# Kernel optimization log

Hardware: AMD Instinct MI355X
Metric: run time of the kernel (lower is better)

The kernel has to match this reference:

```python
import jax, jax.numpy as jnp
import numpy as np

HEADS = 6
POINTS = 4
INJ_SHAPES = ((96, 96), (48, 48), (24, 24))  # adapter pyramid (H_l, W_l), sum = 12096 tokens
EXT_SHAPES = ((48, 48),)                      # vit grid level


def layernorm(x, g, b, eps=1e-6):
    m = jnp.mean(x, axis=-1, keepdims=True)
    v = jnp.mean((x - m) ** 2, axis=-1, keepdims=True)
    return (x - m) * jax.lax.rsqrt(v + eps) * g + b


def bilinear_sample(img, loc):
    # img: [B, heads, H, W, D]; loc: [B, heads, P, 2] normalized (x, y) in [0, 1]
    # matches F.grid_sample(mode='bilinear', padding_mode='zeros', align_corners=False)
    B, nh, H, W, D = img.shape
    flat = img.reshape(B, nh, H * W, D)
    ix = loc[..., 0] * W - 0.5
    iy = loc[..., 1] * H - 0.5
    x0f = jnp.floor(ix)
    y0f = jnp.floor(iy)
    wx = (ix - x0f)[..., None]
    wy = (iy - y0f)[..., None]
    x0 = x0f.astype(jnp.int32)
    y0 = y0f.astype(jnp.int32)

    def gather(xi, yi):
        valid = (xi >= 0) & (xi < W) & (yi >= 0) & (yi < H)
        idx = jnp.clip(yi, 0, H - 1) * W + jnp.clip(xi, 0, W - 1)
        g = jnp.take_along_axis(flat, idx[..., None], axis=2)
        return g * valid[..., None]

    v00 = gather(x0, y0)
    v01 = gather(x0 + 1, y0)
    v10 = gather(x0, y0 + 1)
    v11 = gather(x0 + 1, y0 + 1)
    return (v00 * (1 - wx) + v01 * wx) * (1 - wy) + (v10 * (1 - wx) + v11 * wx) * wy


def msda(query, value, ref, shapes, Wv, bv, Ws, bs_, Wa, ba, Wo, bo):
    # mmcv MultiScaleDeformableAttention (batch_first) without dropout/identity.
    B, Lq, C = query.shape
    D = C // HEADS
    L = len(shapes)
    v = (value @ Wv + bv).reshape(B, -1, HEADS, D)
    off = (query @ Ws + bs_).reshape(B, Lq, HEADS, L, POINTS, 2)
    aw = jax.nn.softmax((query @ Wa + ba).reshape(B, Lq, HEADS, L * POINTS), axis=-1)
    aw = aw.reshape(B, Lq, HEADS, L, POINTS)
    norm = jnp.array([[w, h] for (h, w) in shapes], dtype=query.dtype)  # (x, y) normalizer
    # ref: [B, Lq, 1, 2] broadcasts over heads/levels/points
    loc = ref[:, :, None, :, None, :] + off / norm[None, None, None, :, None, :]
    starts = np.cumsum([0] + [h * w for h, w in shapes])
    out = jnp.zeros((B, HEADS, Lq, D), query.dtype)
    for l, (h, w) in enumerate(shapes):
        vl = v[:, starts[l]:starts[l + 1]].reshape(B, h, w, HEADS, D).transpose(0, 3, 1, 2, 4)
        ll = loc[:, :, :, l].transpose(0, 2, 1, 3, 4).reshape(B, HEADS, Lq * POINTS, 2)
        s = bilinear_sample(vl, ll).reshape(B, HEADS, Lq, POINTS, D)
        out = out + jnp.einsum('bhqp,bhqpd->bhqd', aw[:, :, :, l].transpose(0, 2, 1, 3), s)
    out = out.transpose(0, 2, 1, 3).reshape(B, Lq, C)
    return out @ Wo + bo


def setup_inputs() -> dict:
    key = jax.random.key(0)
    ks = jax.random.split(key, 24)
    B, Hh, Ww, C = 1, 48, 48, 768
    NA = 12096  # 4*HW + HW + HW/4
    f32 = jnp.float32
    lin = lambda k, i, o, s=0.02: jax.random.normal(k, (i, o), f32) * s
    p = {
        'vit_feats': jax.random.normal(ks[0], (B, Hh, Ww, C), f32),
        'adapter_feats': jax.random.normal(ks[1], (B, NA, C), f32),
        'ref1': jax.random.uniform(ks[2], (B, Hh * Ww, 1, 2), f32),
        'ref2': jax.random.uniform(ks[3], (B, NA, 1, 2), f32),
        'inj_qn_g': jnp.ones((C,), f32), 'inj_qn_b': jnp.zeros((C,), f32),
        'inj_Wv': lin(ks[4], C, C), 'inj_bv': jnp.zeros((C,), f32),
        'inj_Ws': lin(ks[5], C, HEADS * 3 * POINTS * 2, 0.01),
        'inj_bs': jax.random.normal(ks[6], (HEADS * 3 * POINTS * 2,), f32),
        'inj_Wa': lin(ks[7], C, HEADS * 3 * POINTS), 'inj_ba': jnp.zeros((HEADS * 3 * POINTS,), f32),
        'inj_Wo': lin(ks[8], C, C), 'inj_bo': jnp.zeros((C,), f32),
        'inj_gamma': jax.random.normal(ks[9], (C,), f32) * 0.1,
        'ext_vn_g': jnp.ones((C,), f32), 'ext_vn_b': jnp.zeros((C,), f32),
        'ext_qn_g': jnp.ones((C,), f32), 'ext_qn_b': jnp.zeros((C,), f32),
        'ext_Wv': lin(ks[10], C, C), 'ext_bv': jnp.zeros((C,), f32),
        'ext_Ws': lin(ks[11], C, HEADS * 1 * POINTS * 2, 0.01),
        'ext_bs': jax.random.normal(ks[12], (HEADS * 1 * POINTS * 2,), f32),
        'ext_Wa': lin(ks[13], C, HEADS * 1 * POINTS), 'ext_ba': jnp.zeros((HEADS * 1 * POINTS,), f32),
        'ext_Wo': lin(ks[14], C, C), 'ext_bo': jnp.zeros((C,), f32),
        'H': 48, 'W': 48,
    }
    return p


def reference(vit_feats, adapter_feats, ref1, ref2,
              inj_qn_g, inj_qn_b, inj_Wv, inj_bv, inj_Ws, inj_bs, inj_Wa, inj_ba, inj_Wo, inj_bo, inj_gamma,
              ext_vn_g, ext_vn_b, ext_qn_g, ext_qn_b, ext_Wv, ext_bv, ext_Ws, ext_bs, ext_Wa, ext_ba, ext_Wo, ext_bo,
              H, W):
    b, h, w, c = vit_feats.shape
    q = vit_feats.reshape(b, h * w, c)
    # Injector: query = vit tokens, value = 3-level adapter pyramid; identity = 0, gamma-scaled residual
    attn = msda(layernorm(q, inj_qn_g, inj_qn_b), adapter_feats, ref1, INJ_SHAPES,
                inj_Wv, inj_bv, inj_Ws, inj_bs, inj_Wa, inj_ba, inj_Wo, inj_bo)
    q = q + inj_gamma * attn
    vit_out = q.reshape(b, h, w, c)
    # Extractor (with_cffn=False, v_pre_norm=True): value = LN(vit tokens), identity = adapter query, post query-norm
    value = layernorm(q, ext_vn_g, ext_vn_b)
    attn2 = msda(adapter_feats, value, ref2, EXT_SHAPES,
                 ext_Wv, ext_bv, ext_Ws, ext_bs, ext_Wa, ext_ba, ext_Wo, ext_bo)
    adapter_out = layernorm(adapter_feats + attn2, ext_qn_g, ext_qn_b)
    return vit_out, adapter_out
```

## Files before the change

kernel.cpp:

```cpp
#include <hip/hip_runtime.h>


#define LQ_VIT 2304
#define NA_ADA 12096

typedef float f32x4 __attribute__((ext_vector_type(4)));
typedef short bf16x8 __attribute__((ext_vector_type(8)));

__device__ __forceinline__ unsigned short f2bf(float f) {
  unsigned u = __builtin_bit_cast(unsigned, f);
  u += 0x7FFFu + ((u >> 16) & 1u);
  return (unsigned short)(u >> 16);
}
__device__ __forceinline__ float bf2f(unsigned short u) {
  return __builtin_bit_cast(float, (unsigned)u << 16);
}
__device__ __forceinline__ f32x4 ld4bf(const unsigned short* p) {
  ushort4 t = *(const ushort4*)p;
  f32x4 r; r[0] = bf2f(t.x); r[1] = bf2f(t.y); r[2] = bf2f(t.z); r[3] = bf2f(t.w);
  return r;
}

__device__ __forceinline__ void gload_lds16(const void* g, void* l) {
  __builtin_amdgcn_global_load_lds(
      (__attribute__((address_space(1))) void*)(void*)g,
      (__attribute__((address_space(3))) void*)l, 16, 0, 0);
}

#define FENCE() __builtin_amdgcn_sched_barrier(0)

struct PrepPack {
  const float* W[8];
  unsigned short* WT[8];
  int N[8];
  int cum[9];
  const float* adapter; unsigned short* adbf; int n4;
  const float* vit; const float* qg; const float* qb; unsigned short* qln;
  const float* isv; const float* iav; const float* ibv;
  const float* esv; const float* eav;
  float* bci; float* bbig;
};

__global__ __launch_bounds__(256) void prep_kernel(PrepPack pp) {
  int b = blockIdx.x;
  int tid = threadIdx.x;
  if (b < 2568) {
    int kb = b / 107, col = b % 107;
    int z = 0;
#pragma unroll
    for (int i = 0; i < 8; i++) if (col >= pp.cum[i + 1]) z = i + 1;
    int nb = col - pp.cum[z];
    const float* __restrict__ W = pp.W[z];
    unsigned short* __restrict__ WT = pp.WT[z];
    int N = pp.N[z];
    int kb32 = kb * 32, nb32 = nb * 32;
    __shared__ float tile[32][33];
    int tx = tid & 31, ty = tid >> 5;
    for (int i = ty; i < 32; i += 8) {
      int n = nb32 + tx;
      tile[i][tx] = (n < N) ? W[(size_t)(kb32 + i) * N + n] : 0.f;
    }
    __syncthreads();
    for (int i = ty; i < 32; i += 8) {
      int n = nb32 + i, k = kb32 + tx;
      if (n < N) WT[(size_t)n * 768 + k] = f2bf(tile[tx][i]);
    }
  } else if (b < 4616) {
    for (int i = (b - 2568) * 256 + tid; i < pp.n4; i += 2048 * 256) {
      float4 v = ((const float4*)pp.adapter)[i];
      ushort4 o;
      o.x = f2bf(v.x); o.y = f2bf(v.y); o.z = f2bf(v.z); o.w = f2bf(v.w);
      ((ushort4*)pp.adbf)[i] = o;
    }
  } else if (b < 5192) {
    int wid = (b - 4616) * 4 + (tid >> 6);
    int lane = tid & 63;
    if (wid >= LQ_VIT) return;
    const float* row = pp.vit + (size_t)wid * 768;
    float x[12]; float s = 0.f;
#pragma unroll
    for (int j = 0; j < 12; j++) { x[j] = row[lane + j * 64]; s += x[j]; }
#pragma unroll
    for (int o = 32; o >= 1; o >>= 1) s += __shfl_xor(s, o);
    float mean = s * (1.f / 768.f);
    float v = 0.f;
#pragma unroll
    for (int j = 0; j < 12; j++) { float d = x[j] - mean; v += d * d; }
#pragma unroll
    for (int o = 32; o >= 1; o >>= 1) v += __shfl_xor(v, o);
    float rs = rsqrtf(v * (1.f / 768.f) + 1e-6f);
#pragma unroll
    for (int j = 0; j < 12; j++) {
      int c = lane + j * 64;
      pp.qln[(size_t)wid * 768 + c] = f2bf((x[j] - mean) * rs * pp.qg[c] + pp.qb[c]);
    }
  } else {
    for (int i = tid; i < 840; i += 256) {
      if (i < 144) pp.bci[i] = pp.isv[i];
      else if (i < 216) pp.bci[i] = pp.iav[i - 144];
      if (i < 768) pp.bbig[i] = pp.ibv[i];
      else if (i < 816) pp.bbig[i] = pp.esv[i - 768];
      else pp.bbig[i] = pp.eav[i - 816];
    }
  }
}

struct GemmTask {
  const unsigned short* A; const unsigned short* BT;
  const float* bias; unsigned short* C;
  int M, N, NT, nwg;
};

__global__ __launch_bounds__(256) void gemm_big_kernel(GemmTask t0, GemmTask t1, int split) {
  __shared__ unsigned short lds[3][(128 + 128) * 32];

  GemmTask tk = (blockIdx.x < split) ? t0 : t1;
  int id = (blockIdx.x < split) ? blockIdx.x : blockIdx.x - split;
  int nwg = tk.nwg;
  int qq = nwg >> 3, rr = nwg & 7;
  int xcd = id & 7, idx = id >> 3;
  int wg = (xcd < rr ? xcd * (qq + 1) : rr * (qq + 1) + (xcd - rr) * qq) + idx;
  int nt = wg % tk.NT, mt = wg / tk.NT;
  int m0 = mt * 128, n0 = nt * 128;
  int M = tk.M, N = tk.N;
  const unsigned short* __restrict__ A = tk.A;
  const unsigned short* __restrict__ BT = tk.BT;
  const int K = 768, kT = 24;

  int tid = threadIdx.x;
  int w = tid >> 6, lane = tid & 63;
  int wr = w >> 1, wc = w & 1;
  int frow = lane & 15, ghi = lane >> 4;
  int sr = lane >> 2;
  int sgx = (((lane & 3) ^ ((lane >> 3) & 3)) * 8);
  int gxr = ((ghi ^ ((frow >> 1) & 3)) * 8);

  f32x4 acc[4][4] = {};

  auto stage = [&](unsigned short* dst, int k0) {
#pragma unroll
    for (int i = 0; i < 4; i++) {
      int c = w * 4 + i;
      if (c < 8) {
        int gm = m0 + c * 16 + sr; if (gm >= M) gm = M - 1;
        gload_lds16(&A[(size_t)gm * K + k0 + sgx], &dst[c * 512]);
      } else {
        int gn = n0 + (c - 8) * 16 + sr; if (gn >= N) gn = N - 1;
        gload_lds16(&BT[(size_t)gn * K + k0 + sgx], &dst[c * 512]);
      }
    }
  };

  stage(&lds[0][0], 0);
  stage(&lds[1][0], 32);
  asm volatile("s_waitcnt vmcnt(4)" ::: "memory");
  FENCE();
  __builtin_amdgcn_s_barrier();
  FENCE();

#pragma unroll
  for (int t = 0; t < kT; t++) {
    unsigned short* cb = &lds[t % 3][0];
    if (t + 2 < kT) stage(&lds[(t + 2) % 3][0], (t + 2) << 5);
    const unsigned short* As_ = cb;
    const unsigned short* Bs_ = cb + 128 * 32;
    bf16x8 af[4], bg[4];
#pragma unroll
    for (int m = 0; m < 4; m++)
      af[m] = *(const bf16x8*)&As_[(wr * 64 + m * 16 + frow) * 32 + gxr];
#pragma unroll
    for (int n = 0; n < 4; n++)
      bg[n] = *(const bf16x8*)&Bs_[(wc * 64 + n * 16 + frow) * 32 + gxr];
#pragma unroll
    for (int m = 0; m < 4; m++)
#pragma unroll
      for (int n = 0; n < 4; n++)
        acc[m][n] = __builtin_amdgcn_mfma_f32_16x16x32_bf16(af[m], bg[n], acc[m][n], 0, 0, 0);
    if (t < kT - 1) {
      if (t + 2 < kT) { asm volatile("s_waitcnt vmcnt(4)" ::: "memory"); }
      else            { asm volatile("s_waitcnt vmcnt(0)" ::: "memory"); }
      FENCE();
      __builtin_amdgcn_s_barrier();
      FENCE();
    }
  }

  int orow = (lane >> 4) * 4, ocol = lane & 15;
  unsigned short* C = tk.C;
  const float* bias = tk.bias;
#pragma unroll
  for (int m = 0; m < 4; m++) {
    int gmb = m0 + wr * 64 + m * 16 + orow;
#pragma unroll
    for (int n = 0; n < 4; n++) {
      int gn = n0 + wc * 64 + n * 16 + ocol;
      if (gn < N) {
        float bv = bias[gn];
#pragma unroll
        for (int r = 0; r < 4; r++) {
          int gm = gmb + r;
          if (gm < M) C[(size_t)gm * N + gn] = f2bf(acc[m][n][r] + bv);
        }
      }
    }
  }
}

__global__ __launch_bounds__(256) void gemm_mid_kernel(
    const unsigned short* __restrict__ A, const unsigned short* __restrict__ BT,
    const float* __restrict__ bias, unsigned short* __restrict__ C,
    int M, int N, int NT) {
  __shared__ unsigned short lds[3][(64 + 128) * 32];

  int nwg = gridDim.x;
  int id = blockIdx.x;
  int qq = nwg >> 3, rr = nwg & 7;
  int xcd = id & 7, idx = id >> 3;
  int wg = (xcd < rr ? xcd * (qq + 1) : rr * (qq + 1) + (xcd - rr) * qq) + idx;
  int nt = wg % NT, mt = wg / NT;
  int m0 = mt * 64, n0 = nt * 128;
  const int K = 768, kT = 24;

  int tid = threadIdx.x;
  int w = tid >> 6, lane = tid & 63;
  int frow = lane & 15, ghi = lane >> 4;
  int sr = lane >> 2;
  int sgx = (((lane & 3) ^ ((lane >> 3) & 3)) * 8);
  int gxr = ((ghi ^ ((frow >> 1) & 3)) * 8);

  f32x4 acc[4][2] = {};

  auto stage = [&](unsigned short* dst, int k0) {
#pragma unroll
    for (int i = 0; i < 3; i++) {
      int c = w * 3 + i;
      if (c < 4) {
        int gm = m0 + c * 16 + sr; if (gm >= M) gm = M - 1;
        gload_lds16(&A[(size_t)gm * K + k0 + sgx], &dst[c * 512]);
      } else {
        int gn = n0 + (c - 4) * 16 + sr; if (gn >= N) gn = N - 1;
        gload_lds16(&BT[(size_t)gn * K + k0 + sgx], &dst[c * 512]);
      }
    }
  };

  stage(&lds[0][0], 0);
  stage(&lds[1][0], 32);
  asm volatile("s_waitcnt vmcnt(3)" ::: "memory");
  FENCE();
  __builtin_amdgcn_s_barrier();
  FENCE();

#pragma unroll
  for (int t = 0; t < kT; t++) {
    unsigned short* cb = &lds[t % 3][0];
    if (t + 2 < kT) stage(&lds[(t + 2) % 3][0], (t + 2) << 5);
    const unsigned short* As_ = cb;
    const unsigned short* Bs_ = cb + 64 * 32;
    bf16x8 af[4], bg[2];
#pragma unroll
    for (int m = 0; m < 4; m++)
      af[m] = *(const bf16x8*)&As_[(m * 16 + frow) * 32 + gxr];
#pragma unroll
    for (int n = 0; n < 2; n++)
      bg[n] = *(const bf16x8*)&Bs_[(w * 32 + n * 16 + frow) * 32 + gxr];
#pragma unroll
    for (int m = 0; m < 4; m++)
#pragma unroll
      for (int n = 0; n < 2; n++)
        acc[m][n] = __builtin_amdgcn_mfma_f32_16x16x32_bf16(af[m], bg[n], acc[m][n], 0, 0, 0);
    if (t < kT - 1) {
      if (t + 2 < kT) { asm volatile("s_waitcnt vmcnt(3)" ::: "memory"); }
      else            { asm volatile("s_waitcnt vmcnt(0)" ::: "memory"); }
      FENCE();
      __builtin_amdgcn_s_barrier();
      FENCE();
    }
  }

  int orow = (lane >> 4) * 4, ocol = lane & 15;
#pragma unroll
  for (int m = 0; m < 4; m++) {
    int gmb = m0 + m * 16 + orow;
#pragma unroll
    for (int n = 0; n < 2; n++) {
      int gn = n0 + w * 32 + n * 16 + ocol;
      if (gn < N) {
        float bv = bias[gn];
#pragma unroll
        for (int r = 0; r < 4; r++) {
          int gm = gmb + r;
          if (gm < M) C[(size_t)gm * N + gn] = f2bf(acc[m][n][r] + bv);
        }
      }
    }
  }
}

__global__ __launch_bounds__(256) void residual_ln_kernel(
    const float* __restrict__ vit, const unsigned short* __restrict__ attn,
    const float* __restrict__ gamma, const float* __restrict__ g,
    const float* __restrict__ b, float* __restrict__ vout,
    unsigned short* __restrict__ vln, int R) {
  int wid = blockIdx.x * 4 + (threadIdx.x >> 6);
  int lane = threadIdx.x & 63;
  if (wid >= R) return;
  const float* ra = vit + (size_t)wid * 768;
  const unsigned short* rb = attn + (size_t)wid * 768;
  float x[12]; float s = 0.f;
#pragma unroll
  for (int j = 0; j < 12; j++) {
    int c = lane + j * 64;
    x[j] = ra[c] + gamma[c] * bf2f(rb[c]);
    vout[(size_t)wid * 768 + c] = x[j];
    s += x[j];
  }
#pragma unroll
  for (int o = 32; o >= 1; o >>= 1) s += __shfl_xor(s, o);
  float mean = s * (1.f / 768.f);
  float v = 0.f;
#pragma unroll
  for (int j = 0; j < 12; j++) { float d = x[j] - mean; v += d * d; }
#pragma unroll
  for (int o = 32; o >= 1; o >>= 1) v += __shfl_xor(v, o);
  float rs = rsqrtf(v * (1.f / 768.f) + 1e-6f);
#pragma unroll
  for (int j = 0; j < 12; j++) {
    int c = lane + j * 64;
    vln[(size_t)wid * 768 + c] = f2bf((x[j] - mean) * rs * g[c] + b[c]);
  }
}

__global__ __launch_bounds__(256) void add_ln_f32_kernel(
    const float* __restrict__ Xa, const unsigned short* __restrict__ Xb,
    const float* __restrict__ g, const float* __restrict__ b,
    float* __restrict__ out, int R) {
  int wid = blockIdx.x * 4 + (threadIdx.x >> 6);
  int lane = threadIdx.x & 63;
  if (wid >= R) return;
  const float* ra = Xa + (size_t)wid * 768;
  const unsigned short* rb = Xb + (size_t)wid * 768;
  float x[12]; float s = 0.f;
#pragma unroll
  for (int j = 0; j < 12; j++) {
    int c = lane + j * 64;
    x[j] = ra[c] + bf2f(rb[c]); s += x[j];
  }
#pragma unroll
  for (int o = 32; o >= 1; o >>= 1) s += __shfl_xor(s, o);
  float mean = s * (1.f / 768.f);
  float v = 0.f;
#pragma unroll
  for (int j = 0; j < 12; j++) { float d = x[j] - mean; v += d * d; }
#pragma unroll
  for (int o = 32; o >= 1; o >>= 1) v += __shfl_xor(v, o);
  float rs = rsqrtf(v * (1.f / 768.f) + 1e-6f);
#pragma unroll
  for (int j = 0; j < 12; j++) {
    int c = lane + j * 64;
    out[(size_t)wid * 768 + c] = (x[j] - mean) * rs * g[c] + b[c];
  }
}

__global__ __launch_bounds__(256) void sampler_inj_kernel(
    const float* __restrict__ ref, const unsigned short* __restrict__ sa,
    const unsigned short* __restrict__ v, unsigned short* __restrict__ out, int vst) {
  int gw = (blockIdx.x * 256 + threadIdx.x) >> 6;
  int lane = threadIdx.x & 63;
  int q = gw / 3, hp = gw - q * 3;
  if (q >= LQ_VIT) return;
  int h = hp * 2 + (lane >> 5);
  int c = h * 128 + (lane & 31) * 4;
  float rx = ref[q * 2], ry = ref[q * 2 + 1];
  const unsigned short* row = sa + (size_t)q * 216;
  float lg[12]; float mx = -1e30f;
#pragma unroll
  for (int i = 0; i < 12; i++) { lg[i] = bf2f(row[144 + h * 12 + i]); mx = fmaxf(mx, lg[i]); }
  float s = 0.f;
#pragma unroll
  for (int i = 0; i < 12; i++) { lg[i] = __expf(lg[i] - mx); s += lg[i]; }
  float inv = 1.f / s;
  f32x4 acc = {0.f, 0.f, 0.f, 0.f};
  const int LW[3] = {96, 48, 24};
  const int LS[3] = {0, 9216, 11520};
#pragma unroll
  for (int l = 0; l < 3; l++) {
    const int Wl = LW[l], st = LS[l], Wm = Wl - 1;
    const float Wf = (float)Wl;
#pragma unroll
    for (int p = 0; p < 4; p++) {
      int ob = ((h * 3 + l) * 4 + p) * 2;
      float ix = fmaf(rx, Wf, bf2f(row[ob])) - 0.5f;
      float iy = fmaf(ry, Wf, bf2f(row[ob + 1])) - 0.5f;
      float x0f = floorf(ix), y0f = floorf(iy);
      float wx = ix - x0f, wy = iy - y0f;
      int x0 = (int)x0f, y0 = (int)y0f;
      float aw = lg[l * 4 + p] * inv;
      float wy0 = (1.f - wy) * aw, wy1 = wy * aw;
      float w00 = (1.f - wx) * wy0, w01 = wx * wy0;
      float w10 = (1.f - wx) * wy1, w11 = wx * wy1;
      bool xv0 = (unsigned)x0 < (unsigned)Wl, xv1 = (unsigned)(x0 + 1) < (unsigned)Wl;
      bool yv0 = (unsigned)y0 < (unsigned)Wl, yv1 = (unsigned)(y0 + 1) < (unsigned)Wl;
      w00 = (xv0 && yv0) ? w00 : 0.f;
      w01 = (xv1 && yv0) ? w01 : 0.f;
      w10 = (xv0 && yv1) ? w10 : 0.f;
      w11 = (xv1 && yv1) ? w11 : 0.f;
      int x0c = min(max(x0, 0), Wm), x1c = min(max(x0 + 1, 0), Wm);
      int y0c = min(max(y0, 0), Wm), y1c = min(max(y0 + 1, 0), Wm);
      const unsigned short* r0 = v + ((size_t)(st + y0c * Wl) * vst + c);
      const unsigned short* r1 = v + ((size_t)(st + y1c * Wl) * vst + c);
      acc += w00 * ld4bf(r0 + (size_t)x0c * vst) + w01 * ld4bf(r0 + (size_t)x1c * vst)
           + w10 * ld4bf(r1 + (size_t)x0c * vst) + w11 * ld4bf(r1 + (size_t)x1c * vst);
    }
  }
  ushort4 o4;
  o4.x = f2bf(acc[0]); o4.y = f2bf(acc[1]); o4.z = f2bf(acc[2]); o4.w = f2bf(acc[3]);
  *(ushort4*)&out[(size_t)q * 768 + c] = o4;
}

__global__ __launch_bounds__(256) void sampler_ext_kernel(
    const float* __restrict__ ref, const unsigned short* __restrict__ sa, int sst,
    const unsigned short* __restrict__ v, unsigned short* __restrict__ out) {
  int gw = (blockIdx.x * 256 + threadIdx.x) >> 6;
  int lane = threadIdx.x & 63;
  int q = gw / 3, hp = gw - q * 3;
  if (q >= NA_ADA) return;
  int h = hp * 2 + (lane >> 5);
  int c = h * 128 + (lane & 31) * 4;
  float rx = ref[q * 2], ry = ref[q * 2 + 1];
  const unsigned short* row = sa + (size_t)q * sst;
  float lg[4]; float mx = -1e30f;
#pragma unroll
  for (int p = 0; p < 4; p++) { lg[p] = bf2f(row[48 + h * 4 + p]); mx = fmaxf(mx, lg[p]); }
  float s = 0.f;
#pragma unroll
  for (int p = 0; p < 4; p++) { lg[p] = __expf(lg[p] - mx); s += lg[p]; }
  float inv = 1.f / s;
  f32x4 acc = {0.f, 0.f, 0.f, 0.f};
#pragma unroll
  for (int p = 0; p < 4; p++) {
    int ob = (h * 4 + p) * 2;
    float ix = fmaf(rx, 48.f, bf2f(row[ob])) - 0.5f;
    float iy = fmaf(ry, 48.f, bf2f(row[ob + 1])) - 0.5f;
    float x0f = floorf(ix), y0f = floorf(iy);
    float wx = ix - x0f, wy = iy - y0f;
    int x0 = (int)x0f, y0 = (int)y0f;
    float aw = lg[p] * inv;
    float wy0 = (1.f - wy) * aw, wy1 = wy * aw;
    float w00 = (1.f - wx) * wy0, w01 = wx * wy0;
    float w10 = (1.f - wx) * wy1, w11 = wx * wy1;
    bool xv0 = (unsigned)x0 < 48u, xv1 = (unsigned)(x0 + 1) < 48u;
    bool yv0 = (unsigned)y0 < 48u, yv1 = (unsigned)(y0 + 1) < 48u;
    w00 = (xv0 && yv0) ? w00 : 0.f;
    w01 = (xv1 && yv0) ? w01 : 0.f;
    w10 = (xv0 && yv1) ? w10 : 0.f;
    w11 = (xv1 && yv1) ? w11 : 0.f;
    int x0c = min(max(x0, 0), 47), x1c = min(max(x0 + 1, 0), 47);
    int y0c = min(max(y0, 0), 47), y1c = min(max(y0 + 1, 0), 47);
    const unsigned short* r0 = v + ((size_t)(y0c * 48) * 768 + c);
    const unsigned short* r1 = v + ((size_t)(y1c * 48) * 768 + c);
    acc += w00 * ld4bf(r0 + (size_t)x0c * 768) + w01 * ld4bf(r0 + (size_t)x1c * 768)
         + w10 * ld4bf(r1 + (size_t)x0c * 768) + w11 * ld4bf(r1 + (size_t)x1c * 768);
  }
  ushort4 o4;
  o4.x = f2bf(acc[0]); o4.y = f2bf(acc[1]); o4.z = f2bf(acc[2]); o4.w = f2bf(acc[3]);
  *(ushort4*)&out[(size_t)q * 768 + c] = o4;
}

extern "C" void kernel_launch(void* const* d_in, const int* in_sizes, int n_in,
                              void* d_out, int out_size, void* d_ws, size_t ws_size,
                              hipStream_t stream) {
  (void)in_sizes; (void)n_in; (void)out_size; (void)ws_size;
  const float* vit      = (const float*)d_in[0];
  const float* adapter  = (const float*)d_in[1];
  const float* ref1     = (const float*)d_in[2];
  const float* ref2     = (const float*)d_in[3];
  const float* inj_qn_g = (const float*)d_in[4];
  const float* inj_qn_b = (const float*)d_in[5];
  const float* inj_Wv   = (const float*)d_in[6];
  const float* inj_bv   = (const float*)d_in[7];
  const float* inj_Ws   = (const float*)d_in[8];
  const float* inj_bs   = (const float*)d_in[9];
  const float* inj_Wa   = (const float*)d_in[10];
  const float* inj_ba   = (const float*)d_in[11];
  const float* inj_Wo   = (const float*)d_in[12];
  const float* inj_bo   = (const float*)d_in[13];
  const float* inj_gamma= (const float*)d_in[14];
  const float* ext_vn_g = (const float*)d_in[15];
  const float* ext_vn_b = (const float*)d_in[16];
  const float* ext_qn_g = (const float*)d_in[17];
  const float* ext_qn_b = (const float*)d_in[18];
  const float* ext_Wv   = (const float*)d_in[19];
  const float* ext_bv   = (const float*)d_in[20];
  const float* ext_Ws   = (const float*)d_in[21];
  const float* ext_bs   = (const float*)d_in[22];
  const float* ext_Wa   = (const float*)d_in[23];
  const float* ext_ba   = (const float*)d_in[24];
  const float* ext_Wo   = (const float*)d_in[25];
  const float* ext_bo   = (const float*)d_in[26];

  size_t cur = 0;
  auto take = [&](size_t bytes) {
    void* p = (char*)d_ws + cur;
    cur += (bytes + 255) & ~(size_t)255;
    return p;
  };
  unsigned short* WBIG = (unsigned short*)take((size_t)840 * 768 * 2);
  unsigned short* WTIO = (unsigned short*)take((size_t)768 * 768 * 2);
  unsigned short* WTEV = (unsigned short*)take((size_t)768 * 768 * 2);
  unsigned short* WTEO = (unsigned short*)take((size_t)768 * 768 * 2);
  unsigned short* WSAI = (unsigned short*)take((size_t)216 * 768 * 2);
  float* BCI  = (float*)take((size_t)216 * 4);
  float* BBIG = (float*)take((size_t)840 * 4);
  unsigned short* ADBF = (unsigned short*)take((size_t)NA_ADA * 768 * 2);
  unsigned short* QLN  = (unsigned short*)take((size_t)LQ_VIT * 768 * 2);
  unsigned short* CBIG = (unsigned short*)take((size_t)NA_ADA * 840 * 2);
  unsigned short* SAI  = (unsigned short*)take((size_t)LQ_VIT * 216 * 2);
  unsigned short* SAMPI= (unsigned short*)take((size_t)LQ_VIT * 768 * 2);
  unsigned short* ATTNI= (unsigned short*)take((size_t)LQ_VIT * 768 * 2);
  unsigned short* VLN  = (unsigned short*)take((size_t)LQ_VIT * 768 * 2);
  unsigned short* VEXT = (unsigned short*)take((size_t)LQ_VIT * 768 * 2);
  unsigned short* SAMPE = ADBF;
  unsigned short* ATTN2 = CBIG;

  float* out_vit = (float*)d_out;
  float* out_ada = out_vit + (size_t)LQ_VIT * 768;

  PrepPack pp;
  pp.W[0] = inj_Wv; pp.WT[0] = WBIG;               pp.N[0] = 768;
  pp.W[1] = ext_Ws; pp.WT[1] = WBIG + 768 * 768;   pp.N[1] = 48;
  pp.W[2] = ext_Wa; pp.WT[2] = WBIG + 816 * 768;   pp.N[2] = 24;
  pp.W[3] = inj_Wo; pp.WT[3] = WTIO;               pp.N[3] = 768;
  pp.W[4] = ext_Wv; pp.WT[4] = WTEV;               pp.N[4] = 768;
  pp.W[5] = ext_Wo; pp.WT[5] = WTEO;               pp.N[5] = 768;
  pp.W[6] = inj_Ws; pp.WT[6] = WSAI;               pp.N[6] = 144;
  pp.W[7] = inj_Wa; pp.WT[7] = WSAI + 144 * 768;   pp.N[7] = 72;
  int cum = 0;
  for (int i = 0; i < 8; i++) { pp.cum[i] = cum; cum += (pp.N[i] + 31) / 32; }
  pp.cum[8] = cum;
  pp.adapter = adapter; pp.adbf = ADBF; pp.n4 = (NA_ADA * 768) / 4;
  pp.vit = vit; pp.qg = inj_qn_g; pp.qb = inj_qn_b; pp.qln = QLN;
  pp.isv = inj_bs; pp.iav = inj_ba; pp.ibv = inj_bv;
  pp.esv = ext_bs; pp.eav = ext_ba;
  pp.bci = BCI; pp.bbig = BBIG;
  prep_kernel<<<5193, 256, 0, stream>>>(pp);

  GemmTask tA, tB;
  tA.A = ADBF; tA.BT = WBIG; tA.bias = BBIG; tA.C = CBIG;
  tA.M = NA_ADA; tA.N = 840; tA.NT = 7; tA.nwg = 95 * 7;
  tB.A = QLN; tB.BT = WSAI; tB.bias = BCI; tB.C = SAI;
  tB.M = LQ_VIT; tB.N = 216; tB.NT = 2; tB.nwg = 18 * 2;
  gemm_big_kernel<<<95 * 7 + 18 * 2, 256, 0, stream>>>(tA, tB, 95 * 7);

  sampler_inj_kernel<<<1728, 256, 0, stream>>>(ref1, SAI, CBIG, SAMPI, 840);

  gemm_mid_kernel<<<36 * 6, 256, 0, stream>>>(SAMPI, WTIO, inj_bo, ATTNI, LQ_VIT, 768, 6);
  residual_ln_kernel<<<576, 256, 0, stream>>>(vit, ATTNI, inj_gamma, ext_vn_g, ext_vn_b,
                                              out_vit, VLN, LQ_VIT);
  gemm_mid_kernel<<<36 * 6, 256, 0, stream>>>(VLN, WTEV, ext_bv, VEXT, LQ_VIT, 768, 6);

  sampler_ext_kernel<<<9072, 256, 0, stream>>>(ref2, CBIG + 768, 840, VEXT, SAMPE);

  GemmTask tC;
  tC.A = SAMPE; tC.BT = WTEO; tC.bias = ext_bo; tC.C = ATTN2;
  tC.M = NA_ADA; tC.N = 768; tC.NT = 6; tC.nwg = 95 * 6;
  gemm_big_kernel<<<95 * 6, 256, 0, stream>>>(tC, tC, 95 * 6);

  add_ln_f32_kernel<<<3024, 256, 0, stream>>>(adapter, ATTN2, ext_qn_g, ext_qn_b, out_ada, NA_ADA);
}
```

Before: 169.0 us.

## Use 8-wave GEMM blocks and 8-channel-per-lane vectorized samplers

The big GEMM now runs 512 threads (8 waves, each computing a 64x32 sub-tile) per 128x128 tile instead of 4 waves with 64x64 sub-tiles. This halves per-wave accumulators and staging loads, so latency hiding and occupancy should improve. Both deformable samplers now have each lane handle 8 channels with 16-byte loads and stores, and each wave covers 4 heads across two queries, halving the grid size. The risks are higher register pressure per lane in the samplers and more barrier contention across 8 waves in the GEMM.

Result: faster. 160.5 us (-5.0%).

```diff
diff --git a/kernel.cpp b/kernel.cpp
--- a/kernel.cpp
+++ b/kernel.cpp
@@ -5,7 +5,9 @@
 #define NA_ADA 12096
 
 typedef float f32x4 __attribute__((ext_vector_type(4)));
+typedef float f32x8 __attribute__((ext_vector_type(8)));
 typedef short bf16x8 __attribute__((ext_vector_type(8)));
+typedef unsigned short u16x8 __attribute__((ext_vector_type(8)));
 
 __device__ __forceinline__ unsigned short f2bf(float f) {
   unsigned u = __builtin_bit_cast(unsigned, f);
@@ -15,9 +17,11 @@
 __device__ __forceinline__ float bf2f(unsigned short u) {
   return __builtin_bit_cast(float, (unsigned)u << 16);
 }
-__device__ __forceinline__ f32x4 ld4bf(const unsigned short* p) {
-  ushort4 t = *(const ushort4*)p;
-  f32x4 r; r[0] = bf2f(t.x); r[1] = bf2f(t.y); r[2] = bf2f(t.z); r[3] = bf2f(t.w);
+__device__ __forceinline__ f32x8 ld8bf(const unsigned short* p) {
+  u16x8 t = *(const u16x8*)p;
+  f32x8 r;
+#pragma unroll
+  for (int j = 0; j < 8; j++) r[j] = bf2f(t[j]);
   return r;
 }
 
@@ -28,6 +32,8 @@
 }
 
 #define FENCE() __builtin_amdgcn_sched_barrier(0)
+#define WAITV(n) do { asm volatile("s_waitcnt vmcnt(" #n ")" ::: "memory"); } while (0)
+#define BAR() do { FENCE(); __builtin_amdgcn_s_barrier(); FENCE(); } while (0)
 
 struct PrepPack {
   const float* W[8];
@@ -111,7 +117,7 @@
   int M, N, NT, nwg;
 };
 
-__global__ __launch_bounds__(256) void gemm_big_kernel(GemmTask t0, GemmTask t1, int split) {
+__global__ __launch_bounds__(512) void gemm_big8_kernel(GemmTask t0, GemmTask t1, int split) {
   __shared__ unsigned short lds[3][(128 + 128) * 32];
 
   GemmTask tk = (blockIdx.x < split) ? t0 : t1;
@@ -129,18 +135,18 @@
 
   int tid = threadIdx.x;
   int w = tid >> 6, lane = tid & 63;
-  int wr = w >> 1, wc = w & 1;
+  int wr = w >> 2, wc = w & 3;
   int frow = lane & 15, ghi = lane >> 4;
   int sr = lane >> 2;
   int sgx = (((lane & 3) ^ ((lane >> 3) & 3)) * 8);
   int gxr = ((ghi ^ ((frow >> 1) & 3)) * 8);
 
-  f32x4 acc[4][4] = {};
+  f32x4 acc[4][2] = {};
 
   auto stage = [&](unsigned short* dst, int k0) {
 #pragma unroll
-    for (int i = 0; i < 4; i++) {
-      int c = w * 4 + i;
+    for (int i = 0; i < 2; i++) {
+      int c = w * 2 + i;
       if (c < 8) {
         int gm = m0 + c * 16 + sr; if (gm >= M) gm = M - 1;
         gload_lds16(&A[(size_t)gm * K + k0 + sgx], &dst[c * 512]);
@@ -153,10 +159,8 @@
 
   stage(&lds[0][0], 0);
   stage(&lds[1][0], 32);
-  asm volatile("s_waitcnt vmcnt(4)" ::: "memory");
-  FENCE();
-  __builtin_amdgcn_s_barrier();
-  FENCE();
+  WAITV(2);
+  BAR();
 
 #pragma unroll
   for (int t = 0; t < kT; t++) {
@@ -164,24 +168,22 @@
     if (t + 2 < kT) stage(&lds[(t + 2) % 3][0], (t + 2) << 5);
     const unsigned short* As_ = cb;
     const unsigned short* Bs_ = cb + 128 * 32;
-    bf16x8 af[4], bg[4];
+    bf16x8 af[4], bg[2];
 #pragma unroll
     for (int m = 0; m < 4; m++)
       af[m] = *(const bf16x8*)&As_[(wr * 64 + m * 16 + frow) * 32 + gxr];
 #pragma unroll
-    for (int n = 0; n < 4; n++)
-      bg[n] = *(const bf16x8*)&Bs_[(wc * 64 + n * 16 + frow) * 32 + gxr];
+    for (int n = 0; n < 2; n++)
+      bg[n] = *(const bf16x8*)&Bs_[(wc * 32 + n * 16 + frow) * 32 + gxr];
 #pragma unroll
     for (int m = 0; m < 4; m++)
 #pragma unroll
-      for (int n = 0; n < 4; n++)
+      for (int n = 0; n < 2; n++)
         acc[m][n] = __builtin_amdgcn_mfma_f32_16x16x32_bf16(af[m], bg[n], acc[m][n], 0, 0, 0);
     if (t < kT - 1) {
-      if (t + 2 < kT) { asm volatile("s_waitcnt vmcnt(4)" ::: "memory"); }
-      else            { asm volatile("s_waitcnt vmcnt(0)" ::: "memory"); }
-      FENCE();
-      __builtin_amdgcn_s_barrier();
-      FENCE();
+      if (t + 2 < kT) { WAITV(2); }
+      else            { WAITV(0); }
+      BAR();
     }
   }
 
@@ -192,8 +194,8 @@
   for (int m = 0; m < 4; m++) {
     int gmb = m0 + wr * 64 + m * 16 + orow;
 #pragma unroll
-    for (int n = 0; n < 4; n++) {
-      int gn = n0 + wc * 64 + n * 16 + ocol;
+    for (int n = 0; n < 2; n++) {
+      int gn = n0 + wc * 32 + n * 16 + ocol;
       if (gn < N) {
         float bv = bias[gn];
 #pragma unroll
@@ -246,10 +248,8 @@
 
   stage(&lds[0][0], 0);
   stage(&lds[1][0], 32);
-  asm volatile("s_waitcnt vmcnt(3)" ::: "memory");
-  FENCE();
-  __builtin_amdgcn_s_barrier();
-  FENCE();
+  WAITV(3);
+  BAR();
 
 #pragma unroll
   for (int t = 0; t < kT; t++) {
@@ -270,11 +270,9 @@
       for (int n = 0; n < 2; n++)
         acc[m][n] = __builtin_amdgcn_mfma_f32_16x16x32_bf16(af[m], bg[n], acc[m][n], 0, 0, 0);
     if (t < kT - 1) {
-      if (t + 2 < kT) { asm volatile("s_waitcnt vmcnt(3)" ::: "memory"); }
-      else            { asm volatile("s_waitcnt vmcnt(0)" ::: "memory"); }
-      FENCE();
-      __builtin_amdgcn_s_barrier();
-      FENCE();
+      if (t + 2 < kT) { WAITV(3); }
+      else            { WAITV(0); }
+      BAR();
     }
   }
 
@@ -362,15 +360,18 @@
   }
 }
 
+
 __global__ __launch_bounds__(256) void sampler_inj_kernel(
     const float* __restrict__ ref, const unsigned short* __restrict__ sa,
     const unsigned short* __restrict__ v, unsigned short* __restrict__ out, int vst) {
   int gw = (blockIdx.x * 256 + threadIdx.x) >> 6;
   int lane = threadIdx.x & 63;
-  int q = gw / 3, hp = gw - q * 3;
+  int qp = gw / 3, wv = gw - qp * 3;
+  int gh = wv * 4 + (lane >> 4);
+  int q = qp * 2 + (gh >= 6 ? 1 : 0);
   if (q >= LQ_VIT) return;
-  int h = hp * 2 + (lane >> 5);
-  int c = h * 128 + (lane & 31) * 4;
+  int h = gh >= 6 ? gh - 6 : gh;
+  int c = h * 128 + (lane & 15) * 8;
   float rx = ref[q * 2], ry = ref[q * 2 + 1];
   const unsigned short* row = sa + (size_t)q * 216;
   float lg[12]; float mx = -1e30f;
@@ -380,7 +381,7 @@
 #pragma unroll
   for (int i = 0; i < 12; i++) { lg[i] = __expf(lg[i] - mx); s += lg[i]; }
   float inv = 1.f / s;
-  f32x4 acc = {0.f, 0.f, 0.f, 0.f};
+  f32x8 acc = {};
   const int LW[3] = {96, 48, 24};
   const int LS[3] = {0, 9216, 11520};
 #pragma unroll
@@ -409,13 +410,14 @@
       int y0c = min(max(y0, 0), Wm), y1c = min(max(y0 + 1, 0), Wm);
       const unsigned short* r0 = v + ((size_t)(st + y0c * Wl) * vst + c);
       const unsigned short* r1 = v + ((size_t)(st + y1c * Wl) * vst + c);
-      acc += w00 * ld4bf(r0 + (size_t)x0c * vst) + w01 * ld4bf(r0 + (size_t)x1c * vst)
-           + w10 * ld4bf(r1 + (size_t)x0c * vst) + w11 * ld4bf(r1 + (size_t)x1c * vst);
-    }
-  }
-  ushort4 o4;
-  o4.x = f2bf(acc[0]); o4.y = f2bf(acc[1]); o4.z = f2bf(acc[2]); o4.w = f2bf(acc[3]);
-  *(ushort4*)&out[(size_t)q * 768 + c] = o4;
+      acc += w00 * ld8bf(r0 + (size_t)x0c * vst) + w01 * ld8bf(r0 + (size_t)x1c * vst)
+           + w10 * ld8bf(r1 + (size_t)x0c * vst) + w11 * ld8bf(r1 + (size_t)x1c * vst);
+    }
+  }
+  u16x8 o8;
+#pragma unroll
+  for (int j = 0; j < 8; j++) o8[j] = f2bf(acc[j]);
+  *(u16x8*)&out[(size_t)q * 768 + c] = o8;
 }
 
 __global__ __launch_bounds__(256) void sampler_ext_kernel(
@@ -423,10 +425,12 @@
     const unsigned short* __restrict__ v, unsigned short* __restrict__ out) {
   int gw = (blockIdx.x * 256 + threadIdx.x) >> 6;
   int lane = threadIdx.x & 63;
-  int q = gw / 3, hp = gw - q * 3;
+  int qp = gw / 3, wv = gw - qp * 3;
+  int gh = wv * 4 + (lane >> 4);
+  int q = qp * 2 + (gh >= 6 ? 1 : 0);
   if (q >= NA_ADA) return;
-  int h = hp * 2 + (lane >> 5);
-  int c = h * 128 + (lane & 31) * 4;
+  int h = gh >= 6 ? gh - 6 : gh;
+  int c = h * 128 + (lane & 15) * 8;
   float rx = ref[q * 2], ry = ref[q * 2 + 1];
   const unsigned short* row = sa + (size_t)q * sst;
   float lg[4]; float mx = -1e30f;
@@ -436,7 +440,7 @@
 #pragma unroll
   for (int p = 0; p < 4; p++) { lg[p] = __expf(lg[p] - mx); s += lg[p]; }
   float inv = 1.f / s;
-  f32x4 acc = {0.f, 0.f, 0.f, 0.f};
+  f32x8 acc = {};
 #pragma unroll
   for (int p = 0; p < 4; p++) {
     int ob = (h * 4 + p) * 2;
@@ -459,12 +463,13 @@
     int y0c = min(max(y0, 0), 47), y1c = min(max(y0 + 1, 0), 47);
     const unsigned short* r0 = v + ((size_t)(y0c * 48) * 768 + c);
     const unsigned short* r1 = v + ((size_t)(y1c * 48) * 768 + c);
-    acc += w00 * ld4bf(r0 + (size_t)x0c * 768) + w01 * ld4bf(r0 + (size_t)x1c * 768)
-         + w10 * ld4bf(r1 + (size_t)x0c * 768) + w11 * ld4bf(r1 + (size_t)x1c * 768);
-  }
-  ushort4 o4;
-  o4.x = f2bf(acc[0]); o4.y = f2bf(acc[1]); o4.z = f2bf(acc[2]); o4.w = f2bf(acc[3]);
-  *(ushort4*)&out[(size_t)q * 768 + c] = o4;
+    acc += w00 * ld8bf(r0 + (size_t)x0c * 768) + w01 * ld8bf(r0 + (size_t)x1c * 768)
+         + w10 * ld8bf(r1 + (size_t)x0c * 768) + w11 * ld8bf(r1 + (size_t)x1c * 768);
+  }
+  u16x8 o8;
+#pragma unroll
+  for (int j = 0; j < 8; j++) o8[j] = f2bf(acc[j]);
+  *(u16x8*)&out[(size_t)q * 768 + c] = o8;
 }
 
 extern "C" void kernel_launch(void* const* d_in, const int* in_sizes, int n_in,
@@ -550,21 +555,21 @@
   tA.M = NA_ADA; tA.N = 840; tA.NT = 7; tA.nwg = 95 * 7;
   tB.A = QLN; tB.BT = WSAI; tB.bias = BCI; tB.C = SAI;
   tB.M = LQ_VIT; tB.N = 216; tB.NT = 2; tB.nwg = 18 * 2;
-  gemm_big_kernel<<<95 * 7 + 18 * 2, 256, 0, stream>>>(tA, tB, 95 * 7);
-
-  sampler_inj_kernel<<<1728, 256, 0, stream>>>(ref1, SAI, CBIG, SAMPI, 840);
+  gemm_big8_kernel<<<95 * 7 + 18 * 2, 512, 0, stream>>>(tA, tB, 95 * 7);
+
+  sampler_inj_kernel<<<864, 256, 0, stream>>>(ref1, SAI, CBIG, SAMPI, 840);
 
   gemm_mid_kernel<<<36 * 6, 256, 0, stream>>>(SAMPI, WTIO, inj_bo, ATTNI, LQ_VIT, 768, 6);
   residual_ln_kernel<<<576, 256, 0, stream>>>(vit, ATTNI, inj_gamma, ext_vn_g, ext_vn_b,
                                               out_vit, VLN, LQ_VIT);
   gemm_mid_kernel<<<36 * 6, 256, 0, stream>>>(VLN, WTEV, ext_bv, VEXT, LQ_VIT, 768, 6);
 
-  sampler_ext_kernel<<<9072, 256, 0, stream>>>(ref2, CBIG + 768, 840, VEXT, SAMPE);
+  sampler_ext_kernel<<<4536, 256, 0, stream>>>(ref2, CBIG + 768, 840, VEXT, SAMPE);
 
   GemmTask tC;
   tC.A = SAMPE; tC.BT = WTEO; tC.bias = ext_bo; tC.C = ATTN2;
   tC.M = NA_ADA; tC.N = 768; tC.NT = 6; tC.nwg = 95 * 6;
-  gemm_big_kernel<<<95 * 6, 256, 0, stream>>>(tC, tC, 95 * 6);
+  gemm_big8_kernel<<<95 * 6, 512, 0, stream>>>(tC, tC, 95 * 6);
 
   add_ln_f32_kernel<<<3024, 256, 0, stream>>>(adapter, ATTN2, ext_qn_g, ext_qn_b, out_ada, NA_ADA);
 }
```
